# Performance work log

Measured on AMD Instinct MI355X. Metric: run time of the kernel, lower is better.

Reference implementation:

```python
import jax, jax.numpy as jnp
import numpy as np

N_OBJ, N_EVT, N_EDGE, N_MAIN = 50000, 100000, 500000, 25000
OBJ_DIM, EVT_DIM = 256, 256


def setup_inputs() -> dict:
    key = jax.random.key(0)
    ks = jax.random.split(key, 12)
    s = 1.0 / np.sqrt(OBJ_DIM)
    return {
        "object_X": jax.random.normal(ks[0], (N_OBJ, OBJ_DIM), jnp.float32),
        "event_X": jax.random.normal(ks[1], (N_EVT, EVT_DIM), jnp.float32),
        "lc_obj_idx": jax.random.randint(ks[2], (N_EDGE,), 0, N_OBJ),
        "lc_evt_idx": jax.random.randint(ks[3], (N_EDGE,), 0, N_EVT),
        "main_idx": jax.random.randint(ks[4], (N_MAIN,), 0, N_OBJ),
        # lifecycle_proj: Linear(event_dim, obj_dim)
        "W_proj": jax.random.uniform(ks[5], (OBJ_DIM, EVT_DIM), jnp.float32, -s, s),
        "b_proj": jax.random.uniform(ks[6], (OBJ_DIM,), jnp.float32, -s, s),
        # GRUCell(obj_dim, obj_dim): weight_ih/hh are [3*H, H]
        "W_ih": jax.random.uniform(ks[7], (3 * OBJ_DIM, OBJ_DIM), jnp.float32, -s, s),
        "b_ih": jax.random.uniform(ks[8], (3 * OBJ_DIM,), jnp.float32, -s, s),
        "W_hh": jax.random.uniform(ks[9], (3 * OBJ_DIM, OBJ_DIM), jnp.float32, -s, s),
        "b_hh": jax.random.uniform(ks[10], (3 * OBJ_DIM,), jnp.float32, -s, s),
    }


def reference(object_X, event_X, lc_obj_idx, lc_evt_idx, main_idx,
              W_proj, b_proj, W_ih, b_ih, W_hh, b_hh):
    n_obj = object_X.shape[0]
    # gather event feats, linear + ReLU  -> [E, obj_dim]
    proj = jax.nn.relu(event_X[lc_evt_idx] @ W_proj.T + b_proj)
    # scatter_mean over target objects (empty slots -> 0, like torch_scatter)
    sums = jax.ops.segment_sum(proj, lc_obj_idx, num_segments=n_obj)
    cnt = jax.ops.segment_sum(jnp.ones((lc_obj_idx.shape[0],), proj.dtype),
                              lc_obj_idx, num_segments=n_obj)
    profile = sums / jnp.maximum(cnt, 1.0)[:, None]  # [N_obj, obj_dim]
    # GRUCell(profile, object_X)
    gi = profile @ W_ih.T + b_ih   # [N_obj, 3H]
    gh = object_X @ W_hh.T + b_hh  # [N_obj, 3H]
    i_r, i_z, i_n = jnp.split(gi, 3, axis=-1)
    h_r, h_z, h_n = jnp.split(gh, 3, axis=-1)
    r = jax.nn.sigmoid(i_r + h_r)
    z = jax.nn.sigmoid(i_z + h_z)
    n = jnp.tanh(i_n + r * h_n)
    updated = (1.0 - z) * n + z * object_X
    # masked blend: only main objects take updated values
    mask = jnp.zeros((n_obj, 1), object_X.dtype).at[main_idx].set(1.0)
    return mask * updated + (1.0 - mask) * object_X
```

## Files before the change

kernel.cpp:

```cpp
#include <hip/hip_runtime.h>

typedef unsigned short u16;
typedef __attribute__((ext_vector_type(8))) short bf16x8;
typedef __attribute__((ext_vector_type(4))) float f32x4;

struct __align__(8) u16x4_t { u16 x, y, z, w; };

__device__ __forceinline__ float b2f(u16 b) {
  union { unsigned u; float f; } v; v.u = ((unsigned)b) << 16; return v.f;
}
__device__ __forceinline__ u16 f2b(float f) {
  union { float f; unsigned u; } v; v.f = f;
  unsigned r = v.u + 0x7fffu + ((v.u >> 16) & 1u);
  return (u16)(r >> 16);
}

__global__ void prep(const float* __restrict__ evtX, u16* __restrict__ evtb, int nEvtF4,
                     const float* __restrict__ Wp, const float* __restrict__ Wi,
                     const float* __restrict__ Wh, u16* __restrict__ wb,
                     const int* __restrict__ main_idx, int* __restrict__ mask,
                     int* __restrict__ mlist, int* __restrict__ cpos,
                     int* __restrict__ mcount, int nMain) {
  const int cvtBlocks = nEvtF4 / 256;
  int b = blockIdx.x;
  if (b < cvtBlocks) {
    int t = b * 256 + threadIdx.x;
    float4 v = ((const float4*)evtX)[t];
    u16x4_t o;
    o.x = f2b(v.x); o.y = f2b(v.y); o.z = f2b(v.z); o.w = f2b(v.w);
    ((u16x4_t*)evtb)[t] = o;
  } else if (b < cvtBlocks + 448) {
    int t = (b - cvtBlocks) * 256 + threadIdx.x;
    const float* src; int o;
    if (t < 16384)      { src = Wp; o = t; }
    else if (t < 65536) { src = Wi; o = t - 16384; }
    else                { src = Wh; o = t - 65536; }
    float4 v = ((const float4*)src)[o];
    u16x4_t q;
    q.x = f2b(v.x); q.y = f2b(v.y); q.z = f2b(v.z); q.w = f2b(v.w);
    ((u16x4_t*)wb)[t] = q;
  } else {
    int t = (b - cvtBlocks - 448) * 256 + threadIdx.x;
    if (t < nMain) {
      int o = main_idx[t];
      if (atomicCAS(&mask[o], 0, 1) == 0) {
        int i = atomicAdd(mcount, 1);
        mlist[i] = o;
        cpos[o] = i;
      }
    }
  }
}

__global__ void count_edges(const int* __restrict__ obj_idx, const int* __restrict__ mask,
                            int* __restrict__ deg, int n) {
  int e = blockIdx.x * 256 + threadIdx.x;
  if (e >= n) return;
  int o = obj_idx[e];
  if (mask[o]) atomicAdd(&deg[o], 1);
}

__global__ __launch_bounds__(256)
void alloc_offs(const int* __restrict__ mlist, const int* __restrict__ mcount,
                const int* __restrict__ deg, int* __restrict__ offs,
                int* __restrict__ tcur, int* __restrict__ rrows, int Mpad) {
  int i = blockIdx.x * 256 + threadIdx.x;
  int lane = threadIdx.x & 63;
  int mc = *mcount;
  if (i < Mpad) rrows[i] = (i < mc) ? mlist[i] : 0;
  int o = (i < mc) ? mlist[i] : 0;
  int d = (i < mc) ? deg[o] : 0;
  int x = d;
#pragma unroll
  for (int s = 1; s < 64; s <<= 1) {
    int y = __shfl_up(x, s, 64);
    if (lane >= s) x += y;
  }
  int wt = __shfl(x, 63, 64);
  int base = 0;
  if (lane == 63 && wt > 0) base = atomicAdd(tcur, wt);
  base = __shfl(base, 63, 64);
  if (i < mc) offs[o] = base + (x - d);
}

__global__ void fill_edges(const int* __restrict__ obj_idx, const int* __restrict__ evt_idx,
                           const int* __restrict__ mask, const int* __restrict__ offs,
                           int* __restrict__ cursor, int* __restrict__ elist, int n) {
  int e = blockIdx.x * 256 + threadIdx.x;
  if (e >= n) return;
  int o = obj_idx[e];
  if (!mask[o]) return;
  int pos = atomicAdd(&cursor[o], 1);
  elist[offs[o] + pos] = evt_idx[e];
}

__global__ __launch_bounds__(256)
void accum_gather(const u16* __restrict__ P, const int* __restrict__ elist,
                  const int* __restrict__ offs, const int* __restrict__ deg,
                  const int* __restrict__ mlist, const int* __restrict__ mcount,
                  const float* __restrict__ objX, const int* __restrict__ rrows,
                  u16* __restrict__ prof, u16* __restrict__ objc, int Mpad) {
  const int wave = threadIdx.x >> 6;
  const int lane = threadIdx.x & 63;
  const int i = blockIdx.x * 4 + wave;
  if (i >= Mpad) return;

  int src = rrows[i];
  float4 xv = *(const float4*)(objX + (size_t)src * 256 + lane * 4);

  const int mc = *mcount;
  float a0 = 0.f, a1 = 0.f, a2 = 0.f, a3 = 0.f;
  int d = 0;
  if (i < mc) {
    const int o = mlist[i];
    const int off = offs[o];
    d = deg[o];
    int j = 0;
    for (; j + 1 < d; j += 2) {
      int e0 = elist[off + j], e1 = elist[off + j + 1];
      u16x4_t p0 = *(const u16x4_t*)(P + (size_t)e0 * 256 + lane * 4);
      u16x4_t p1 = *(const u16x4_t*)(P + (size_t)e1 * 256 + lane * 4);
      a0 += b2f(p0.x) + b2f(p1.x);
      a1 += b2f(p0.y) + b2f(p1.y);
      a2 += b2f(p0.z) + b2f(p1.z);
      a3 += b2f(p0.w) + b2f(p1.w);
    }
    if (j < d) {
      int e0 = elist[off + j];
      u16x4_t p0 = *(const u16x4_t*)(P + (size_t)e0 * 256 + lane * 4);
      a0 += b2f(p0.x); a1 += b2f(p0.y); a2 += b2f(p0.z); a3 += b2f(p0.w);
    }
  }
  float s = 1.f / fmaxf((float)d, 1.f);
  u16x4_t pv;
  pv.x = f2b(a0 * s); pv.y = f2b(a1 * s); pv.z = f2b(a2 * s); pv.w = f2b(a3 * s);
  *(u16x4_t*)(prof + (size_t)i * 256 + lane * 4) = pv;

  u16x4_t ov;
  ov.x = f2b(xv.x); ov.y = f2b(xv.y); ov.z = f2b(xv.z); ov.w = f2b(xv.w);
  *(u16x4_t*)(objc + (size_t)i * 256 + lane * 4) = ov;
}

template<int RELU>
__device__ __forceinline__
void gemm_core(const u16* __restrict__ A, const u16* __restrict__ B,
               const float* __restrict__ bias, u16* __restrict__ C,
               int M, int N, int n0, u16* lA, u16* lB) {
  const int tid  = threadIdx.x;
  const int lane = tid & 63;
  const int wave = tid >> 6;
  const int m0 = blockIdx.x * 128;
  const int mR = (wave & 1) * 64;
  const int nC = (wave >> 1) * 64;

  f32x4 acc[4][4] = {};

  for (int kt = 0; kt < 256; kt += 64) {
    __syncthreads();
#pragma unroll
    for (int s = 0; s < 4; ++s) {
      int slot = s * 256 + tid;
      int row  = slot >> 3;
      int kk   = (slot & 7) * 8;
      int ar = m0 + row; ar = (ar < M) ? ar : (M - 1);
      const u16* gA = A + (size_t)ar * 256 + (kt + kk);
      __builtin_amdgcn_global_load_lds(
          (const __attribute__((address_space(1))) void*)gA,
          (__attribute__((address_space(3))) void*)(lA + s * 2048 + wave * 512),
          16, 0, 0);
      const u16* gB = B + (size_t)(n0 + row) * 256 + (kt + kk);
      __builtin_amdgcn_global_load_lds(
          (const __attribute__((address_space(1))) void*)gB,
          (__attribute__((address_space(3))) void*)(lB + s * 2048 + wave * 512),
          16, 0, 0);
    }
    __syncthreads();

#pragma unroll
    for (int ks = 0; ks < 2; ++ks) {
      const int kb = ks * 32 + (lane >> 4) * 8;
      bf16x8 af[4], bfr[4];
#pragma unroll
      for (int i = 0; i < 4; ++i) {
        af[i]  = *(const bf16x8*)(lA + (mR + i * 16 + (lane & 15)) * 64 + kb);
        bfr[i] = *(const bf16x8*)(lB + (nC + i * 16 + (lane & 15)) * 64 + kb);
      }
#pragma unroll
      for (int i = 0; i < 4; ++i)
#pragma unroll
        for (int j = 0; j < 4; ++j)
          acc[i][j] = __builtin_amdgcn_mfma_f32_16x16x32_bf16(af[i], bfr[j], acc[i][j], 0, 0, 0);
    }
  }

  const int crow = (lane >> 4) * 4;
  const int ccol = lane & 15;
#pragma unroll
  for (int i = 0; i < 4; ++i) {
#pragma unroll
    for (int j = 0; j < 4; ++j) {
      int col = n0 + nC + j * 16 + ccol;
      float bv = bias[col];
#pragma unroll
      for (int q = 0; q < 4; ++q) {
        int row = m0 + mR + i * 16 + crow + q;
        if (row < M) {
          float v = acc[i][j][q] + bv;
          if (RELU) v = fmaxf(v, 0.f);
          C[(size_t)row * N + col] = f2b(v);
        }
      }
    }
  }
}

__global__ __launch_bounds__(256, 2)
void gemm_p(const u16* __restrict__ A, const u16* __restrict__ B,
            const float* __restrict__ bias, u16* __restrict__ C, int M) {
  __shared__ u16 lA[128 * 64];
  __shared__ u16 lB[128 * 64];
  gemm_core<1>(A, B, bias, C, M, 256, blockIdx.y * 128, lA, lB);
}

__global__ __launch_bounds__(256, 2)
void gemm2_dual(const u16* __restrict__ prof, const u16* __restrict__ objc,
                const u16* __restrict__ wib, const u16* __restrict__ whb,
                const float* __restrict__ bi, const float* __restrict__ bh,
                u16* __restrict__ gi, u16* __restrict__ gh, int Mpad) {
  __shared__ u16 lA[128 * 64];
  __shared__ u16 lB[128 * 64];
  int y = blockIdx.y;
  if (y < 6) gemm_core<0>(prof, wib, bi, gi, Mpad, 768, y * 128, lA, lB);
  else       gemm_core<0>(objc, whb, bh, gh, Mpad, 768, (y - 6) * 128, lA, lB);
}

__global__ __launch_bounds__(256)
void gate_out(const u16* __restrict__ gi, const u16* __restrict__ gh,
              const float* __restrict__ objX, const int* __restrict__ mask,
              const int* __restrict__ cpos, float* __restrict__ out, int nObj) {
  const int wave = threadIdx.x >> 6;
  const int lane = threadIdx.x & 63;
  const int row = blockIdx.x * 4 + wave;
  if (row >= nObj) return;
  float4 x4 = *(const float4*)(objX + (size_t)row * 256 + lane * 4);
  float4 r4 = x4;
  if (mask[row]) {
    size_t b = (size_t)cpos[row] * 768 + lane * 4;
    u16x4_t ir = *(const u16x4_t*)(gi + b);
    u16x4_t iz = *(const u16x4_t*)(gi + b + 256);
    u16x4_t in_ = *(const u16x4_t*)(gi + b + 512);
    u16x4_t hr = *(const u16x4_t*)(gh + b);
    u16x4_t hz = *(const u16x4_t*)(gh + b + 256);
    u16x4_t hn = *(const u16x4_t*)(gh + b + 512);
    float xs[4] = {x4.x, x4.y, x4.z, x4.w};
    u16 irs[4] = {ir.x, ir.y, ir.z, ir.w};
    u16 izs[4] = {iz.x, iz.y, iz.z, iz.w};
    u16 ins[4] = {in_.x, in_.y, in_.z, in_.w};
    u16 hrs[4] = {hr.x, hr.y, hr.z, hr.w};
    u16 hzs[4] = {hz.x, hz.y, hz.z, hz.w};
    u16 hns[4] = {hn.x, hn.y, hn.z, hn.w};
    float rs[4];
#pragma unroll
    for (int q = 0; q < 4; ++q) {
      float r = 1.f / (1.f + __expf(-(b2f(irs[q]) + b2f(hrs[q]))));
      float z = 1.f / (1.f + __expf(-(b2f(izs[q]) + b2f(hzs[q]))));
      float a = b2f(ins[q]) + r * b2f(hns[q]);
      float n = 1.f - 2.f / (__expf(2.f * a) + 1.f);
      rs[q] = (1.f - z) * n + z * xs[q];
    }
    r4.x = rs[0]; r4.y = rs[1]; r4.z = rs[2]; r4.w = rs[3];
  }
  *(float4*)(out + (size_t)row * 256 + lane * 4) = r4;
}


extern "C" void kernel_launch(void* const* d_in, const int* in_sizes, int n_in,
                              void* d_out, int out_size, void* d_ws, size_t ws_size,
                              hipStream_t stream) {
  const float* objX   = (const float*)d_in[0];
  const float* evtX   = (const float*)d_in[1];
  const int* obj_idx  = (const int*)d_in[2];
  const int* evt_idx  = (const int*)d_in[3];
  const int* main_idx = (const int*)d_in[4];
  const float* Wp = (const float*)d_in[5];
  const float* bp = (const float*)d_in[6];
  const float* Wi = (const float*)d_in[7];
  const float* bi = (const float*)d_in[8];
  const float* Wh = (const float*)d_in[9];
  const float* bh = (const float*)d_in[10];

  const int nObj  = in_sizes[0] / 256;
  const int nEvt  = in_sizes[1] / 256;
  const int nEdge = in_sizes[2];
  const int nMain = in_sizes[4];
  const int Mpad  = ((nMain + 127) / 128) * 128;

  char* ws = (char*)d_ws;
  u16*   P     = (u16*)(ws + 0);
  u16*   gi    = (u16*)(ws + 0);
  u16*   gh    = (u16*)(ws + 51200000);
  u16*   prof  = (u16*)(ws + 89735168);
  u16*   objc  = (u16*)(ws + 102580224);
  u16*   evtb  = (u16*)(ws + 115425280);
  u16*   wb    = (u16*)(ws + 166625280);
  u16*   wpb   = wb;
  u16*   wib   = wb + 65536;
  u16*   whb   = wb + 262144;
  int*   deg   = (int*)(ws + 167542784);
  int*   cursor= (int*)(ws + 167742784);
  int*   mask  = (int*)(ws + 167942784);
  int*   mcount= (int*)(ws + 168142784);
  int*   tcur  = (int*)(ws + 168142848);
  int*   cpos  = (int*)(ws + 168142912);
  int*   offs  = (int*)(ws + 168342912);
  int*   mlist = (int*)(ws + 168542912);
  int*   rrows = (int*)(ws + 168643264);
  int*   elist = (int*)(ws + 168743616);
  float* out   = (float*)d_out;

  hipMemsetAsync(ws + 167542784, 0, 600128, stream);

  const int nEvtF4 = in_sizes[1] / 4;
  const int prepGrid = nEvtF4 / 256 + 448 + (nMain + 255) / 256;
  prep<<<prepGrid, 256, 0, stream>>>(evtX, evtb, nEvtF4, Wp, Wi, Wh, wb,
                                     main_idx, mask, mlist, cpos, mcount, nMain);

  gemm_p<<<dim3((nEvt + 127) / 128, 2), 256, 0, stream>>>(evtb, wpb, bp, P, nEvt);

  count_edges<<<(nEdge + 255) / 256, 256, 0, stream>>>(obj_idx, mask, deg, nEdge);
  alloc_offs<<<Mpad / 256, 256, 0, stream>>>(mlist, mcount, deg, offs, tcur, rrows, Mpad);
  fill_edges<<<(nEdge + 255) / 256, 256, 0, stream>>>(obj_idx, evt_idx, mask, offs, cursor, elist, nEdge);

  accum_gather<<<(Mpad + 3) / 4, 256, 0, stream>>>(P, elist, offs, deg, mlist, mcount,
                                                   objX, rrows, prof, objc, Mpad);

  gemm2_dual<<<dim3(Mpad / 128, 12), 256, 0, stream>>>(prof, objc, wib, whb, bi, bh, gi, gh, Mpad);

  gate_out<<<(nObj + 3) / 4, 256, 0, stream>>>(gi, gh, objX, mask, cpos, out, nObj);
}
```

Measured before the change: 379.3 us.

## Load GEMM fragments directly from global memory and remap workgroups per XCD

```diff
diff --git a/kernel.cpp b/kernel.cpp
--- a/kernel.cpp
+++ b/kernel.cpp
@@ -145,52 +145,37 @@
 __device__ __forceinline__
 void gemm_core(const u16* __restrict__ A, const u16* __restrict__ B,
                const float* __restrict__ bias, u16* __restrict__ C,
-               int M, int N, int n0, u16* lA, u16* lB) {
-  const int tid  = threadIdx.x;
-  const int lane = tid & 63;
-  const int wave = tid >> 6;
-  const int m0 = blockIdx.x * 128;
+               int M, int N, int n0, int m0) {
+  const int lane = threadIdx.x & 63;
+  const int wave = threadIdx.x >> 6;
   const int mR = (wave & 1) * 64;
   const int nC = (wave >> 1) * 64;
+  const int lr = lane & 15;
+  const int koff = (lane >> 4) * 8;
+
+  const u16* pa[4];
+  const u16* pb[4];
+#pragma unroll
+  for (int i = 0; i < 4; ++i) {
+    int ar = m0 + mR + i * 16 + lr;
+    ar = (ar < M) ? ar : (M - 1);
+    pa[i] = A + (size_t)ar * 256 + koff;
+    pb[i] = B + (size_t)(n0 + nC + i * 16 + lr) * 256 + koff;
+  }
 
   f32x4 acc[4][4] = {};
-
-  for (int kt = 0; kt < 256; kt += 64) {
-    __syncthreads();
-#pragma unroll
-    for (int s = 0; s < 4; ++s) {
-      int slot = s * 256 + tid;
-      int row  = slot >> 3;
-      int kk   = (slot & 7) * 8;
-      int ar = m0 + row; ar = (ar < M) ? ar : (M - 1);
-      const u16* gA = A + (size_t)ar * 256 + (kt + kk);
-      __builtin_amdgcn_global_load_lds(
-          (const __attribute__((address_space(1))) void*)gA,
-          (__attribute__((address_space(3))) void*)(lA + s * 2048 + wave * 512),
-          16, 0, 0);
-      const u16* gB = B + (size_t)(n0 + row) * 256 + (kt + kk);
-      __builtin_amdgcn_global_load_lds(
-          (const __attribute__((address_space(1))) void*)gB,
-          (__attribute__((address_space(3))) void*)(lB + s * 2048 + wave * 512),
-          16, 0, 0);
-    }
-    __syncthreads();
-
-#pragma unroll
-    for (int ks = 0; ks < 2; ++ks) {
-      const int kb = ks * 32 + (lane >> 4) * 8;
-      bf16x8 af[4], bfr[4];
-#pragma unroll
-      for (int i = 0; i < 4; ++i) {
-        af[i]  = *(const bf16x8*)(lA + (mR + i * 16 + (lane & 15)) * 64 + kb);
-        bfr[i] = *(const bf16x8*)(lB + (nC + i * 16 + (lane & 15)) * 64 + kb);
-      }
-#pragma unroll
-      for (int i = 0; i < 4; ++i)
-#pragma unroll
-        for (int j = 0; j < 4; ++j)
-          acc[i][j] = __builtin_amdgcn_mfma_f32_16x16x32_bf16(af[i], bfr[j], acc[i][j], 0, 0, 0);
-    }
+#pragma unroll
+  for (int kt = 0; kt < 256; kt += 32) {
+    bf16x8 af[4], bf[4];
+#pragma unroll
+    for (int i = 0; i < 4; ++i) af[i] = *(const bf16x8*)(pa[i] + kt);
+#pragma unroll
+    for (int j = 0; j < 4; ++j) bf[j] = *(const bf16x8*)(pb[j] + kt);
+#pragma unroll
+    for (int i = 0; i < 4; ++i)
+#pragma unroll
+      for (int j = 0; j < 4; ++j)
+        acc[i][j] = __builtin_amdgcn_mfma_f32_16x16x32_bf16(af[i], bf[j], acc[i][j], 0, 0, 0);
   }
 
   const int crow = (lane >> 4) * 4;
@@ -214,24 +199,25 @@
   }
 }
 
-__global__ __launch_bounds__(256, 2)
+__global__ __launch_bounds__(256, 3)
 void gemm_p(const u16* __restrict__ A, const u16* __restrict__ B,
             const float* __restrict__ bias, u16* __restrict__ C, int M) {
-  __shared__ u16 lA[128 * 64];
-  __shared__ u16 lB[128 * 64];
-  gemm_core<1>(A, B, bias, C, M, 256, blockIdx.y * 128, lA, lB);
-}
-
-__global__ __launch_bounds__(256, 2)
+  gemm_core<1>(A, B, bias, C, M, 256, blockIdx.y * 128, blockIdx.x * 128);
+}
+
+__global__ __launch_bounds__(256, 3)
 void gemm2_dual(const u16* __restrict__ prof, const u16* __restrict__ objc,
                 const u16* __restrict__ wib, const u16* __restrict__ whb,
                 const float* __restrict__ bi, const float* __restrict__ bh,
-                u16* __restrict__ gi, u16* __restrict__ gh, int Mpad) {
-  __shared__ u16 lA[128 * 64];
-  __shared__ u16 lB[128 * 64];
-  int y = blockIdx.y;
-  if (y < 6) gemm_core<0>(prof, wib, bi, gi, Mpad, 768, y * 128, lA, lB);
-  else       gemm_core<0>(objc, whb, bh, gh, Mpad, 768, (y - 6) * 128, lA, lB);
+                u16* __restrict__ gi, u16* __restrict__ gh, int Mpad, int nwg) {
+  int bid = blockIdx.x;
+  int q = nwg >> 3, r = nwg & 7;
+  int xcd = bid & 7, loc = bid >> 3;
+  int wg = (xcd < r ? xcd * (q + 1) : r * (q + 1) + (xcd - r) * q) + loc;
+  int m0 = (wg / 12) * 128;
+  int y = wg % 12;
+  if (y < 6) gemm_core<0>(prof, wib, bi, gi, Mpad, 768, y * 128, m0);
+  else       gemm_core<0>(objc, whb, bh, gh, Mpad, 768, (y - 6) * 128, m0);
 }
 
 __global__ __launch_bounds__(256)
@@ -334,7 +320,8 @@
   accum_gather<<<(Mpad + 3) / 4, 256, 0, stream>>>(P, elist, offs, deg, mlist, mcount,
                                                    objX, rrows, prof, objc, Mpad);
 
-  gemm2_dual<<<dim3(Mpad / 128, 12), 256, 0, stream>>>(prof, objc, wib, whb, bi, bh, gi, gh, Mpad);
+  const int nwg = (Mpad / 128) * 12;
+  gemm2_dual<<<nwg, 256, 0, stream>>>(prof, objc, wib, whb, bi, bh, gi, gh, Mpad, nwg);
 
   gate_out<<<(nObj + 3) / 4, 256, 0, stream>>>(gi, gh, objX, mask, cpos, out, nObj);
 }
```

Result: slower. 449.1 us (+18.4%).

## Double-buffer GEMM LDS tiles, XOR-swizzle LDS layout, and remap blocks across XCDs

Applied to the files above, without the earlier changes.

```diff
diff --git a/kernel.cpp b/kernel.cpp
--- a/kernel.cpp
+++ b/kernel.cpp
@@ -145,52 +145,67 @@
 __device__ __forceinline__
 void gemm_core(const u16* __restrict__ A, const u16* __restrict__ B,
                const float* __restrict__ bias, u16* __restrict__ C,
-               int M, int N, int n0, u16* lA, u16* lB) {
+               int M, int N, int n0, int m0, u16* lA, u16* lB) {
   const int tid  = threadIdx.x;
   const int lane = tid & 63;
   const int wave = tid >> 6;
-  const int m0 = blockIdx.x * 128;
   const int mR = (wave & 1) * 64;
   const int nC = (wave >> 1) * 64;
 
+  int srow[4], skq[4];
+#pragma unroll
+  for (int s = 0; s < 4; ++s) {
+    int g = s * 256 + tid;
+    srow[s] = g >> 3;
+    skq[s]  = ((g & 7) ^ ((g >> 3) & 7)) << 3;
+  }
+
   f32x4 acc[4][4] = {};
 
-  for (int kt = 0; kt < 256; kt += 64) {
-    __syncthreads();
+  auto STAGE = [&](int buf, int kt) {
 #pragma unroll
     for (int s = 0; s < 4; ++s) {
-      int slot = s * 256 + tid;
-      int row  = slot >> 3;
-      int kk   = (slot & 7) * 8;
+      int row = srow[s];
       int ar = m0 + row; ar = (ar < M) ? ar : (M - 1);
-      const u16* gA = A + (size_t)ar * 256 + (kt + kk);
+      const u16* gA = A + (size_t)ar * 256 + kt + skq[s];
       __builtin_amdgcn_global_load_lds(
           (const __attribute__((address_space(1))) void*)gA,
-          (__attribute__((address_space(3))) void*)(lA + s * 2048 + wave * 512),
+          (__attribute__((address_space(3))) void*)(lA + buf * 8192 + s * 2048 + wave * 512),
           16, 0, 0);
-      const u16* gB = B + (size_t)(n0 + row) * 256 + (kt + kk);
+      const u16* gB = B + (size_t)(n0 + row) * 256 + kt + skq[s];
       __builtin_amdgcn_global_load_lds(
           (const __attribute__((address_space(1))) void*)gB,
-          (__attribute__((address_space(3))) void*)(lB + s * 2048 + wave * 512),
+          (__attribute__((address_space(3))) void*)(lB + buf * 8192 + s * 2048 + wave * 512),
           16, 0, 0);
     }
+  };
+
+  STAGE(0, 0);
+  __syncthreads();
+
+  for (int t = 0; t < 4; ++t) {
+    const int cur = t & 1;
+    if (t < 3) STAGE(cur ^ 1, (t + 1) * 64);
+    const u16* bA = lA + cur * 8192;
+    const u16* bB = lB + cur * 8192;
+#pragma unroll
+    for (int ks = 0; ks < 2; ++ks) {
+      const int kbq = ks * 4 + (lane >> 4);
+      bf16x8 af[4], bf[4];
+#pragma unroll
+      for (int i = 0; i < 4; ++i) {
+        int ra = mR + i * 16 + (lane & 15);
+        af[i] = *(const bf16x8*)(bA + ra * 64 + ((kbq ^ (ra & 7)) << 3));
+        int rb = nC + i * 16 + (lane & 15);
+        bf[i] = *(const bf16x8*)(bB + rb * 64 + ((kbq ^ (rb & 7)) << 3));
+      }
+#pragma unroll
+      for (int i = 0; i < 4; ++i)
+#pragma unroll
+        for (int j = 0; j < 4; ++j)
+          acc[i][j] = __builtin_amdgcn_mfma_f32_16x16x32_bf16(af[i], bf[j], acc[i][j], 0, 0, 0);
+    }
     __syncthreads();
-
-#pragma unroll
-    for (int ks = 0; ks < 2; ++ks) {
-      const int kb = ks * 32 + (lane >> 4) * 8;
-      bf16x8 af[4], bfr[4];
-#pragma unroll
-      for (int i = 0; i < 4; ++i) {
-        af[i]  = *(const bf16x8*)(lA + (mR + i * 16 + (lane & 15)) * 64 + kb);
-        bfr[i] = *(const bf16x8*)(lB + (nC + i * 16 + (lane & 15)) * 64 + kb);
-      }
-#pragma unroll
-      for (int i = 0; i < 4; ++i)
-#pragma unroll
-        for (int j = 0; j < 4; ++j)
-          acc[i][j] = __builtin_amdgcn_mfma_f32_16x16x32_bf16(af[i], bfr[j], acc[i][j], 0, 0, 0);
-    }
   }
 
   const int crow = (lane >> 4) * 4;
@@ -214,24 +229,33 @@
   }
 }
 
+__device__ __forceinline__ int xcd_swz(int bid, int nwg) {
+  int q = nwg >> 3, r = nwg & 7;
+  int xcd = bid & 7, loc = bid >> 3;
+  return (xcd < r ? xcd * (q + 1) : r * (q + 1) + (xcd - r) * q) + loc;
+}
+
 __global__ __launch_bounds__(256, 2)
 void gemm_p(const u16* __restrict__ A, const u16* __restrict__ B,
-            const float* __restrict__ bias, u16* __restrict__ C, int M) {
-  __shared__ u16 lA[128 * 64];
-  __shared__ u16 lB[128 * 64];
-  gemm_core<1>(A, B, bias, C, M, 256, blockIdx.y * 128, lA, lB);
+            const float* __restrict__ bias, u16* __restrict__ C, int M, int nwg) {
+  __shared__ u16 lA[2 * 8192];
+  __shared__ u16 lB[2 * 8192];
+  int wg = xcd_swz(blockIdx.x, nwg);
+  gemm_core<1>(A, B, bias, C, M, 256, (wg & 1) * 128, (wg >> 1) * 128, lA, lB);
 }
 
 __global__ __launch_bounds__(256, 2)
 void gemm2_dual(const u16* __restrict__ prof, const u16* __restrict__ objc,
                 const u16* __restrict__ wib, const u16* __restrict__ whb,
                 const float* __restrict__ bi, const float* __restrict__ bh,
-                u16* __restrict__ gi, u16* __restrict__ gh, int Mpad) {
-  __shared__ u16 lA[128 * 64];
-  __shared__ u16 lB[128 * 64];
-  int y = blockIdx.y;
-  if (y < 6) gemm_core<0>(prof, wib, bi, gi, Mpad, 768, y * 128, lA, lB);
-  else       gemm_core<0>(objc, whb, bh, gh, Mpad, 768, (y - 6) * 128, lA, lB);
+                u16* __restrict__ gi, u16* __restrict__ gh, int Mpad, int nwg) {
+  __shared__ u16 lA[2 * 8192];
+  __shared__ u16 lB[2 * 8192];
+  int wg = xcd_swz(blockIdx.x, nwg);
+  int m0 = (wg / 12) * 128;
+  int y = wg % 12;
+  if (y < 6) gemm_core<0>(prof, wib, bi, gi, Mpad, 768, y * 128, m0, lA, lB);
+  else       gemm_core<0>(objc, whb, bh, gh, Mpad, 768, (y - 6) * 128, m0, lA, lB);
 }
 
 __global__ __launch_bounds__(256)
@@ -325,7 +349,8 @@
   prep<<<prepGrid, 256, 0, stream>>>(evtX, evtb, nEvtF4, Wp, Wi, Wh, wb,
                                      main_idx, mask, mlist, cpos, mcount, nMain);
 
-  gemm_p<<<dim3((nEvt + 127) / 128, 2), 256, 0, stream>>>(evtb, wpb, bp, P, nEvt);
+  const int nwgP = ((nEvt + 127) / 128) * 2;
+  gemm_p<<<nwgP, 256, 0, stream>>>(evtb, wpb, bp, P, nEvt, nwgP);
 
   count_edges<<<(nEdge + 255) / 256, 256, 0, stream>>>(obj_idx, mask, deg, nEdge);
   alloc_offs<<<Mpad / 256, 256, 0, stream>>>(mlist, mcount, deg, offs, tcur, rrows, Mpad);
@@ -334,7 +359,8 @@
   accum_gather<<<(Mpad + 3) / 4, 256, 0, stream>>>(P, elist, offs, deg, mlist, mcount,
                                                    objX, rrows, prof, objc, Mpad);
 
-  gemm2_dual<<<dim3(Mpad / 128, 12), 256, 0, stream>>>(prof, objc, wib, whb, bi, bh, gi, gh, Mpad);
+  const int nwg = (Mpad / 128) * 12;
+  gemm2_dual<<<nwg, 256, 0, stream>>>(prof, objc, wib, whb, bi, bh, gi, gh, Mpad, nwg);
 
   gate_out<<<(nObj + 3) / 4, 256, 0, stream>>>(gi, gh, objX, mask, cpos, out, nObj);
 }
```

After: 389.8 us. 1.03x slower.
